# Performance work log

Hardware: AMD Instinct MI355X
Metric: run time of the kernel (lower is better)

Reference implementation:

```python
import jax, jax.numpy as jnp
import numpy as np

# Config (mirrors MarketBDHConfig / BDHConfig defaults used here)
B, T = 2, 512
NUM_ASSETS, IN_FEAT = 93, 4
D = 256          # n_embd
NH = 4           # n_head
MULT = 64        # mlp_internal_dim_multiplier
NL = 6           # n_layer
NI = D * MULT // NH  # per-head internal dim N = 4096
IN_DIM = NUM_ASSETS * IN_FEAT  # 372
ROPE_THETA = 2.0 ** 16
EPS = 1e-5


def _ln(x):
    # LayerNorm over last dim, elementwise_affine=False
    m = jnp.mean(x, axis=-1, keepdims=True)
    v = jnp.mean(jnp.square(x - m), axis=-1, keepdims=True)
    return (x - m) * jax.lax.rsqrt(v + EPS)


def _rope(x, cos, sin):
    # x: [B,NH,T,NI]; cos/sin: [T, NI//2] (broadcast over B,NH)
    x1, x2 = x[..., 0::2], x[..., 1::2]
    out = jnp.stack([x1 * cos - x2 * sin, x1 * sin + x2 * cos], axis=-1)
    return out.reshape(x.shape)


def setup_inputs() -> dict:
    key = jax.random.key(0)
    ks = jax.random.split(key, 9)
    s = 0.02
    return {
        "x": jax.random.normal(ks[0], (B, T, NUM_ASSETS, IN_FEAT), jnp.float32),
        "in_W": jax.random.normal(ks[1], (IN_DIM, D), jnp.float32) * s,
        "in_b": jnp.zeros((D,), jnp.float32),
        "encoder": jax.random.normal(ks[2], (NH, D, NI), jnp.float32) * s,
        "encoder_v": jax.random.normal(ks[3], (NH, D, NI), jnp.float32) * s,
        "decoder": jax.random.normal(ks[4], (NH * NI, D), jnp.float32) * s,
        "head_W": jax.random.normal(ks[5], (D, IN_DIM), jnp.float32) * s,
        "head_b": jnp.zeros((IN_DIM,), jnp.float32),
    }


def reference(x, in_W, in_b, encoder, encoder_v, decoder, head_W, head_b):
    # input projection: [B,T,N,F] -> [B,T,IN_DIM] -> [B,T,D]
    x_flat = x.reshape(B, T, IN_DIM)
    h = _ln(x_flat @ in_W + in_b)  # [B,T,D]

    # RoPE phase tables over the internal (latent) dimension
    freqs = 1.0 / (ROPE_THETA ** (jnp.arange(0, NI, 2, dtype=jnp.float32) / NI))
    phases = jnp.arange(T, dtype=jnp.float32)[:, None] * freqs[None, :]  # [T, NI/2]
    cos, sin = jnp.cos(phases), jnp.sin(phases)

    dec = decoder.reshape(NH, NI, D)  # head-major flatten matches transpose(1,2).reshape

    for _ in range(NL):
        h_res = h
        # encode + relu-sparsify: [B,NH,T,NI]
        h_sparse = jax.nn.relu(jnp.einsum('btd,hdn->bhtn', h, encoder))
        # BDH attention: linear (no softmax), K is Q, is_causal=False -> dense scores
        qr = _rope(h_sparse, cos, sin)
        scores = jnp.einsum('bhtn,bhsn->bhts', qr, qr)  # [B,NH,T,T]
        yKV = jnp.einsum('bhts,bsd->bhtd', scores, h)    # V = h broadcast over heads
        yKV = _ln(yKV)
        y_sparse = jax.nn.relu(jnp.einsum('bhtd,hdn->bhtn', yKV, encoder_v))
        xy_sparse = h_sparse * y_sparse  # multiplicative gating (dropout p=0)
        yMLP = jnp.einsum('bhtn,hnd->btd', xy_sparse, dec)
        h = _ln(h_res + _ln(yMLP))

    pred = (h @ head_W + head_b).reshape(B, T, NUM_ASSETS, IN_FEAT)
    return pred
```

## Files before the change

### kernel.cpp

```cpp
#include <hip/hip_runtime.h>
#include <math.h>

#define B_ 2
#define T_ 512
#define D_ 256
#define NH_ 4
#define NI_ 4096
#define IN_DIM_ 372
#define NL_ 6
#define EPS_ 1e-5f

typedef unsigned short u16;
typedef __attribute__((ext_vector_type(4))) float f32x4;
typedef __attribute__((ext_vector_type(8))) short bf16x8;

__device__ __forceinline__ u16 f2b(float f) {
  union { float f; unsigned u; } v; v.f = f;
  unsigned r = v.u + 0x7fffu + ((v.u >> 16) & 1u);
  return (u16)(r >> 16);
}
__device__ __forceinline__ float b2f(u16 s) {
  union { unsigned u; float f; } v; v.u = ((unsigned)s) << 16;
  return v.f;
}

__device__ __forceinline__ void gload16(const u16* g, u16* l) {
  __builtin_amdgcn_global_load_lds(
      (const __attribute__((address_space(1))) unsigned int*)g,
      (__attribute__((address_space(3))) unsigned int*)l, 16, 0, 0);
}

__device__ __forceinline__ float blkSum256(float v, float* sb4) {
  #pragma unroll
  for (int o = 32; o > 0; o >>= 1) v += __shfl_down(v, o, 64);
  int w = threadIdx.x >> 6;
  __syncthreads();
  if ((threadIdx.x & 63) == 0) sb4[w] = v;
  __syncthreads();
  return sb4[0] + sb4[1] + sb4[2] + sb4[3];
}

__device__ __forceinline__ void gemm128(const u16* __restrict__ A,
                                        const u16* __restrict__ Bt,
                                        int lda, int k0, int k1,
                                        int row0, int col0,
                                        u16* Als, u16* Bls,
                                        f32x4 acc[4][4]) {
  const int tid = threadIdx.x;
  const int lane = tid & 63;
  const int wv = tid >> 6;
  const int wr = (wv >> 1) << 6;
  const int wc = (wv & 1) << 6;
  const int frow = lane & 15;
  const int kg = lane >> 4;
  const int sw = frow & 7;
  #pragma unroll
  for (int m = 0; m < 4; m++)
    #pragma unroll
    for (int n = 0; n < 4; n++) {
      f32x4 z = {0.f, 0.f, 0.f, 0.f};
      acc[m][n] = z;
    }
  for (int k = k0; k < k1; k += 64) {
    #pragma unroll
    for (int i = 0; i < 4; i++) {
      int s = tid + (i << 8);
      int r = s >> 3;
      int c = (((s & 7) ^ (r & 7)) << 3);
      gload16(A + (long)(row0 + r) * lda + k + c, Als + s * 8);
      gload16(Bt + (long)(col0 + r) * lda + k + c, Bls + s * 8);
    }
    __syncthreads();
    #pragma unroll
    for (int kk = 0; kk < 2; kk++) {
      const int slot = ((((kk << 2) + kg) ^ sw) << 3);
      bf16x8 af[4], bfv[4];
      #pragma unroll
      for (int m = 0; m < 4; m++)
        af[m] = *(const bf16x8*)(Als + (wr + m * 16 + frow) * 64 + slot);
      #pragma unroll
      for (int n = 0; n < 4; n++)
        bfv[n] = *(const bf16x8*)(Bls + (wc + n * 16 + frow) * 64 + slot);
      #pragma unroll
      for (int m = 0; m < 4; m++)
        #pragma unroll
        for (int n = 0; n < 4; n++)
          acc[m][n] = __builtin_amdgcn_mfma_f32_16x16x32_bf16(af[m], bfv[n], acc[m][n], 0, 0, 0);
    }
    __syncthreads();
  }
}

#define EPILOG_SETUP \
  const int lane = threadIdx.x & 63; \
  const int wv = threadIdx.x >> 6; \
  const int wr = (wv >> 1) << 6, wc = (wv & 1) << 6;

#define STAGE_HALF(EXPR) \
  if (wr == h * 64) { \
    _Pragma("unroll") \
    for (int m = 0; m < 4; m++) \
      _Pragma("unroll") \
      for (int n = 0; n < 4; n++) \
        _Pragma("unroll") \
        for (int r = 0; r < 4; r++) { \
          int lr = m * 16 + ((lane >> 4) << 2) + r; \
          int lc = wc + n * 16 + (lane & 15); \
          float _a = acc[m][n][r]; \
          smem[lr * 128 + (lc ^ (((lr >> 2) & 7) << 3))] = f2b(EXPR); \
        } \
  } \
  __syncthreads();

__device__ __forceinline__ void storeC_lds(const f32x4 acc[4][4], u16* smem,
                                           u16* Cb, int ldc, int row0, int col0,
                                           int wr, int wc, int lane) {
  const int tid = threadIdx.x;
  #pragma unroll
  for (int h = 0; h < 2; h++) {
    STAGE_HALF(_a)
    #pragma unroll
    for (int i = 0; i < 4; i++) {
      int idx = i * 256 + tid;
      int lr = idx >> 4, ch = idx & 15;
      uint4 v = *(const uint4*)(smem + lr * 128 + ((ch ^ ((lr >> 2) & 7)) << 3));
      *(uint4*)(Cb + (long)(row0 + h * 64 + lr) * ldc + col0 + ch * 8) = v;
    }
    __syncthreads();
  }
}

__global__ __launch_bounds__(256)
void k_cs(unsigned* __restrict__ cs) {
  int idx = blockIdx.x * 256 + threadIdx.x;
  if (idx >= T_ * (NI_ / 2)) return;
  int t = idx >> 11;
  int k = idx & 2047;
  float freq = exp2f(-(float)k * (1.0f / 128.0f));
  float ph = (float)t * freq;
  cs[idx] = (unsigned)f2b(cosf(ph)) | ((unsigned)f2b(sinf(ph)) << 16);
}

__global__ __launch_bounds__(256)
void ktr(const float* __restrict__ src, u16* __restrict__ dst, int R, int C) {
  __shared__ float tile[64][65];
  long zoff = (long)blockIdx.z * R * C;
  int r0 = blockIdx.y * 64, c0 = blockIdx.x * 64;
  int tid = threadIdx.x;
  int tr = tid >> 4, tc4 = (tid & 15) * 4;
  #pragma unroll
  for (int i = 0; i < 4; i++) {
    int r = tr + i * 16;
    f32x4 v = *(const f32x4*)(src + zoff + (long)(r0 + r) * C + c0 + tc4);
    tile[r][tc4 + 0] = v.x; tile[r][tc4 + 1] = v.y;
    tile[r][tc4 + 2] = v.z; tile[r][tc4 + 3] = v.w;
  }
  __syncthreads();
  #pragma unroll
  for (int i = 0; i < 4; i++) {
    int c = tr + i * 16;
    ushort4 o;
    o.x = f2b(tile[tc4 + 0][c]); o.y = f2b(tile[tc4 + 1][c]);
    o.z = f2b(tile[tc4 + 2][c]); o.w = f2b(tile[tc4 + 3][c]);
    *(ushort4*)(dst + zoff + (long)(c0 + c) * R + r0 + tc4) = o;
  }
}

__global__ __launch_bounds__(256)
void k_input(const float* __restrict__ x, const float* __restrict__ W,
             const float* __restrict__ b, float* __restrict__ hf,
             u16* __restrict__ hbf, u16* __restrict__ hT) {
  __shared__ float xr[IN_DIM_];
  __shared__ float sb[4];
  int bt = blockIdx.x;
  int d = threadIdx.x;
  const float* xrow = x + (long)bt * IN_DIM_;
  for (int k = d; k < IN_DIM_; k += 256) xr[k] = xrow[k];
  __syncthreads();
  float acc = b[d];
  for (int k = 0; k < IN_DIM_; k++) acc += xr[k] * W[k * D_ + d];
  float mean = blkSum256(acc, sb) * (1.0f / D_);
  float c = acc - mean;
  float var = blkSum256(c * c, sb) * (1.0f / D_);
  float out = c * rsqrtf(var + EPS_);
  hf[(long)bt * D_ + d] = out;
  hbf[(long)bt * D_ + d] = f2b(out);
  hT[((long)(bt >> 9) * D_ + d) * T_ + (bt & 511)] = f2b(out);
}

__global__ __launch_bounds__(256)
void g_enc(const u16* __restrict__ hbf, const u16* __restrict__ enct,
           const unsigned* __restrict__ cs, u16* __restrict__ qr) {
  __shared__ u16 smem[16384];
  int head = blockIdx.z;
  int row0 = blockIdx.y * 128, col0 = blockIdx.x * 128;
  f32x4 acc[4][4];
  gemm128(hbf, enct + (long)head * NI_ * D_, D_, 0, D_, row0, col0,
          smem, smem + 8192, acc);
  EPILOG_SETUP
  const int tid = threadIdx.x;
  #pragma unroll
  for (int h = 0; h < 2; h++) {
    STAGE_HALF(fmaxf(_a, 0.f))
    #pragma unroll
    for (int i = 0; i < 4; i++) {
      int idx = i * 256 + tid;
      int lr = idx >> 4, ch = idx & 15;
      uint4 v = *(const uint4*)(smem + lr * 128 + ((ch ^ ((lr >> 2) & 7)) << 3));
      int gr = row0 + h * 64 + lr;
      int b = gr >> 9, t = gr & 511;
      int gcol = col0 + ch * 8;
      uint4 csv = *(const uint4*)(cs + (long)t * (NI_ / 2) + (gcol >> 1));
      const unsigned* pv = &v.x; const unsigned* pc = &csv.x;
      unsigned o[4];
      #pragma unroll
      for (int j = 0; j < 4; j++) {
        float v0 = b2f((u16)pv[j]), v1 = b2f((u16)(pv[j] >> 16));
        float cc = b2f((u16)pc[j]), ss = b2f((u16)(pc[j] >> 16));
        o[j] = (unsigned)f2b(v0 * cc - v1 * ss) | ((unsigned)f2b(v0 * ss + v1 * cc) << 16);
      }
      long qri = (((long)(b * NH_ + head)) * T_ + t) * NI_ + gcol;
      *(uint4*)(qr + qri) = make_uint4(o[0], o[1], o[2], o[3]);
    }
    __syncthreads();
  }
}

__global__ __launch_bounds__(256)
void g_scores(const u16* __restrict__ qr, u16* __restrict__ scpb) {
  __shared__ u16 smem[16384];
  int z2 = blockIdx.z;
  int z = z2 >> 2, ks = z2 & 3;
  const u16* A = qr + (long)z * T_ * NI_;
  int row0 = blockIdx.y * 128, col0 = blockIdx.x * 128;
  f32x4 acc[4][4];
  gemm128(A, A, NI_, ks * 1024, ks * 1024 + 1024, row0, col0,
          smem, smem + 8192, acc);
  EPILOG_SETUP
  storeC_lds(acc, smem, scpb + (long)(ks * 8 + z) * T_ * T_, T_, row0, col0, wr, wc, lane);
}

__global__ __launch_bounds__(256)
void g_ykv(const u16* __restrict__ scpb, const u16* __restrict__ hT,
           u16* __restrict__ ykvpb) {
  __shared__ u16 smem[16384];
  u16* Als = smem;
  u16* Bls = smem + 8192;
  int z2 = blockIdx.z;
  int z = z2 >> 2, ks = z2 & 3;
  int b = z >> 2;
  int row0 = blockIdx.y * 128, col0 = blockIdx.x * 128;
  const long SL = (long)8 * T_ * T_;
  const u16* Ab = scpb + (long)z * T_ * T_;
  const u16* Bt = hT + (long)b * D_ * T_;
  const int tid = threadIdx.x;
  const int lane = tid & 63;
  const int wv = tid >> 6;
  const int wr = (wv >> 1) << 6, wc = (wv & 1) << 6;
  const int frow = lane & 15;
  const int kg = lane >> 4;
  const int sw = frow & 7;
  f32x4 acc[4][4];
  #pragma unroll
  for (int m = 0; m < 4; m++)
    #pragma unroll
    for (int n = 0; n < 4; n++) {
      f32x4 zz = {0.f, 0.f, 0.f, 0.f};
      acc[m][n] = zz;
    }
  const int ar = tid >> 1;
  const int ac0 = (tid & 1) << 2;
  for (int k = ks * 128; k < ks * 128 + 128; k += 64) {
    long gb = (long)(row0 + ar) * T_ + k;
    #pragma unroll
    for (int j = 0; j < 4; j++) {
      int jj = ac0 + j;
      long ga = gb + (jj << 3);
      uint4 p0 = *(const uint4*)(Ab + ga);
      uint4 p1 = *(const uint4*)(Ab + SL + ga);
      uint4 p2 = *(const uint4*)(Ab + 2 * SL + ga);
      uint4 p3 = *(const uint4*)(Ab + 3 * SL + ga);
      const unsigned* q0 = &p0.x; const unsigned* q1 = &p1.x;
      const unsigned* q2 = &p2.x; const unsigned* q3 = &p3.x;
      unsigned o[4];
      #pragma unroll
      for (int w = 0; w < 4; w++) {
        float lo = b2f((u16)q0[w]) + b2f((u16)q1[w]) + b2f((u16)q2[w]) + b2f((u16)q3[w]);
        float hi = b2f((u16)(q0[w] >> 16)) + b2f((u16)(q1[w] >> 16)) +
                   b2f((u16)(q2[w] >> 16)) + b2f((u16)(q3[w] >> 16));
        o[w] = (unsigned)f2b(lo) | ((unsigned)f2b(hi) << 16);
      }
      *(uint4*)(Als + ar * 64 + ((jj ^ (ar & 7)) << 3)) = make_uint4(o[0], o[1], o[2], o[3]);
    }
    #pragma unroll
    for (int i = 0; i < 4; i++) {
      int s = tid + (i << 8);
      int r = s >> 3;
      int c = (((s & 7) ^ (r & 7)) << 3);
      gload16(Bt + (long)(col0 + r) * T_ + k + c, Bls + s * 8);
    }
    __syncthreads();
    #pragma unroll
    for (int kk = 0; kk < 2; kk++) {
      const int slot = ((((kk << 2) + kg) ^ sw) << 3);
      bf16x8 af[4], bfv[4];
      #pragma unroll
      for (int m = 0; m < 4; m++)
        af[m] = *(const bf16x8*)(Als + (wr + m * 16 + frow) * 64 + slot);
      #pragma unroll
      for (int n = 0; n < 4; n++)
        bfv[n] = *(const bf16x8*)(Bls + (wc + n * 16 + frow) * 64 + slot);
      #pragma unroll
      for (int m = 0; m < 4; m++)
        #pragma unroll
        for (int n = 0; n < 4; n++)
          acc[m][n] = __builtin_amdgcn_mfma_f32_16x16x32_bf16(af[m], bfv[n], acc[m][n], 0, 0, 0);
    }
    __syncthreads();
  }
  storeC_lds(acc, smem, ykvpb + (long)(ks * 8 + z) * T_ * D_, D_, row0, col0, wr, wc, lane);
}

__global__ __launch_bounds__(256)
void k_lnykv(const u16* __restrict__ ykvpb, u16* __restrict__ ykvb) {
  __shared__ float sb[4];
  int blk = blockIdx.x;
  int d = threadIdx.x;
  const long SL = (long)8 * T_ * D_;
  long base = (long)blk * D_ + d;
  float acc = b2f(ykvpb[base]) + b2f(ykvpb[SL + base]) +
              b2f(ykvpb[2 * SL + base]) + b2f(ykvpb[3 * SL + base]);
  float mean = blkSum256(acc, sb) * (1.0f / D_);
  float c = acc - mean;
  float var = blkSum256(c * c, sb) * (1.0f / D_);
  ykvb[base] = f2b(c * rsqrtf(var + EPS_));
}

__global__ __launch_bounds__(256)
void g_ysp(const u16* __restrict__ ykvb, const u16* __restrict__ encvt,
           const u16* __restrict__ qr, const unsigned* __restrict__ cs,
           u16* __restrict__ xy) {
  __shared__ u16 smem[16384];
  int z = blockIdx.z;
  int b = z >> 2, head = z & 3;
  int row0 = blockIdx.y * 128, col0 = blockIdx.x * 128;
  f32x4 acc[4][4];
  gemm128(ykvb + (long)z * T_ * D_, encvt + (long)head * NI_ * D_, D_,
          0, D_, row0, col0, smem, smem + 8192, acc);
  EPILOG_SETUP
  const int tid = threadIdx.x;
  #pragma unroll
  for (int h = 0; h < 2; h++) {
    STAGE_HALF(fmaxf(_a, 0.f))
    #pragma unroll
    for (int i = 0; i < 4; i++) {
      int idx = i * 256 + tid;
      int lr = idx >> 4, ch = idx & 15;
      uint4 v = *(const uint4*)(smem + lr * 128 + ((ch ^ ((lr >> 2) & 7)) << 3));
      int t = row0 + h * 64 + lr;
      int gcol = col0 + ch * 8;
      uint4 qv = *(const uint4*)(qr + ((long)z * T_ + t) * NI_ + gcol);
      uint4 csv = *(const uint4*)(cs + (long)t * (NI_ / 2) + (gcol >> 1));
      const unsigned* pv = &v.x; const unsigned* pq = &qv.x; const unsigned* pc = &csv.x;
      unsigned o[4];
      #pragma unroll
      for (int j = 0; j < 4; j++) {
        float v0 = b2f((u16)pv[j]), v1 = b2f((u16)(pv[j] >> 16));
        float q0 = b2f((u16)pq[j]), q1 = b2f((u16)(pq[j] >> 16));
        float cc = b2f((u16)pc[j]), ss = b2f((u16)(pc[j] >> 16));
        float hs0 = fmaxf(cc * q0 + ss * q1, 0.f);
        float hs1 = fmaxf(cc * q1 - ss * q0, 0.f);
        o[j] = (unsigned)f2b(hs0 * v0) | ((unsigned)f2b(hs1 * v1) << 16);
      }
      long xyi = ((long)b * T_ + t) * (NH_ * NI_) + head * NI_ + gcol;
      *(uint4*)(xy + xyi) = make_uint4(o[0], o[1], o[2], o[3]);
    }
    __syncthreads();
  }
}

__global__ __launch_bounds__(256)
void g_ymlp(const u16* __restrict__ xy, const u16* __restrict__ dect,
            u16* __restrict__ ymlppb) {
  __shared__ u16 smem[16384];
  int ks = blockIdx.z;
  int row0 = blockIdx.y * 128, col0 = blockIdx.x * 128;
  f32x4 acc[4][4];
  gemm128(xy, dect, NH_ * NI_, ks * 1024, ks * 1024 + 1024, row0, col0,
          smem, smem + 8192, acc);
  EPILOG_SETUP
  storeC_lds(acc, smem, ymlppb + (long)ks * (B_ * T_) * D_, D_, row0, col0, wr, wc, lane);
}

__global__ __launch_bounds__(256)
void k_dln(const u16* __restrict__ ymlppb, float* __restrict__ hf,
           u16* __restrict__ hbf, u16* __restrict__ hT) {
  __shared__ float sb[4];
  int bt = blockIdx.x;
  int d = threadIdx.x;
  const long SL = (long)(B_ * T_) * D_;
  float acc = 0.f;
  #pragma unroll
  for (int p = 0; p < 16; p++)
    acc += b2f(ymlppb[p * SL + (long)bt * D_ + d]);
  float mean = blkSum256(acc, sb) * (1.0f / D_);
  float c = acc - mean;
  float var = blkSum256(c * c, sb) * (1.0f / D_);
  float u = c * rsqrtf(var + EPS_);
  float v2 = hf[(long)bt * D_ + d] + u;
  float m2 = blkSum256(v2, sb) * (1.0f / D_);
  float c2 = v2 - m2;
  float va2 = blkSum256(c2 * c2, sb) * (1.0f / D_);
  float out = c2 * rsqrtf(va2 + EPS_);
  hf[(long)bt * D_ + d] = out;
  hbf[(long)bt * D_ + d] = f2b(out);
  hT[((long)(bt >> 9) * D_ + d) * T_ + (bt & 511)] = f2b(out);
}

__global__ __launch_bounds__(384)
void k_head(const float* __restrict__ h, const float* __restrict__ W,
            const float* __restrict__ bb, float* __restrict__ out) {
  __shared__ float hr[D_];
  int bt = blockIdx.x;
  int j = threadIdx.x;
  for (int k = j; k < D_; k += 384) hr[k] = h[(long)bt * D_ + k];
  __syncthreads();
  if (j < IN_DIM_) {
    float acc = bb[j];
    for (int d2 = 0; d2 < D_; d2++) acc += hr[d2] * W[(long)d2 * IN_DIM_ + j];
    out[(long)bt * IN_DIM_ + j] = acc;
  }
}

extern "C" void kernel_launch(void* const* d_in, const int* in_sizes, int n_in,
                              void* d_out, int out_size, void* d_ws, size_t ws_size,
                              hipStream_t stream) {
  const float* x    = (const float*)d_in[0];
  const float* in_W = (const float*)d_in[1];
  const float* in_b = (const float*)d_in[2];
  const float* enc  = (const float*)d_in[3];
  const float* encv = (const float*)d_in[4];
  const float* dec  = (const float*)d_in[5];
  const float* hW   = (const float*)d_in[6];
  const float* hb   = (const float*)d_in[7];
  float* out = (float*)d_out;

  char* p = (char*)d_ws;
  auto alloc = [&](size_t bytes) { char* r = p; p += (bytes + 255) & ~(size_t)255; return r; };
  unsigned* cs   = (unsigned*)alloc((size_t)T_ * (NI_ / 2) * 4);
  float* hf      = (float*)alloc((size_t)B_ * T_ * D_ * 4);
  u16*   hbf     = (u16*)  alloc((size_t)B_ * T_ * D_ * 2);
  u16*   hT      = (u16*)  alloc((size_t)B_ * D_ * T_ * 2);
  u16*   enct    = (u16*)  alloc((size_t)NH_ * D_ * NI_ * 2);
  u16*   encvt   = (u16*)  alloc((size_t)NH_ * D_ * NI_ * 2);
  u16*   dect    = (u16*)  alloc((size_t)NH_ * NI_ * D_ * 2);
  u16*   qr      = (u16*)  alloc((size_t)B_ * NH_ * T_ * NI_ * 2);
  u16*   xy      = (u16*)  alloc((size_t)B_ * T_ * NH_ * NI_ * 2);
  u16*   scpb    = (u16*)  alloc((size_t)4 * 8 * T_ * T_ * 2);
  u16*   ykvpb   = (u16*)  alloc((size_t)4 * 8 * T_ * D_ * 2);
  u16*   ykvb    = (u16*)  alloc((size_t)8 * T_ * D_ * 2);
  u16*   ymlppb  = (u16*)  alloc((size_t)16 * B_ * T_ * D_ * 2);

  k_cs<<<dim3(4096), dim3(256), 0, stream>>>(cs);
  ktr<<<dim3(NI_ / 64, D_ / 64, NH_), dim3(256), 0, stream>>>(enc, enct, D_, NI_);
  ktr<<<dim3(NI_ / 64, D_ / 64, NH_), dim3(256), 0, stream>>>(encv, encvt, D_, NI_);
  ktr<<<dim3(D_ / 64, (NH_ * NI_) / 64, 1), dim3(256), 0, stream>>>(dec, dect, NH_ * NI_, D_);
  k_input<<<dim3(B_ * T_), dim3(256), 0, stream>>>(x, in_W, in_b, hf, hbf, hT);

  for (int l = 0; l < NL_; l++) {
    g_enc<<<dim3(32, 8, 4), dim3(256), 0, stream>>>(hbf, enct, cs, qr);
    g_scores<<<dim3(4, 4, 32), dim3(256), 0, stream>>>(qr, scpb);
    g_ykv<<<dim3(2, 4, 32), dim3(256), 0, stream>>>(scpb, hT, ykvpb);
    k_lnykv<<<dim3(B_ * NH_ * T_), dim3(256), 0, stream>>>(ykvpb, ykvb);
    g_ysp<<<dim3(32, 4, 8), dim3(256), 0, stream>>>(ykvb, encvt, qr, cs, xy);
    g_ymlp<<<dim3(2, 8, 16), dim3(256), 0, stream>>>(xy, dect, ymlppb);
    k_dln<<<dim3(B_ * T_), dim3(256), 0, stream>>>(ymlppb, hf, hbf, hT);
  }

  k_head<<<dim3(B_ * T_), dim3(384), 0, stream>>>(hf, hW, hb, out);
}
```

Measured before the change: 798.4 us.

## Double-buffer GEMM LDS, exploit score symmetry, wave-level layernorms, merge transposes

The shared GEMM core now double-buffers its LDS tiles, issuing the next k-slice's global-to-LDS loads before computing on the current one. The scores GEMM computes only the upper-triangular 128x128 tiles of the symmetric Q·Qᵀ and writes each off-diagonal tile again in transposed form. The two layernorm kernels switch to one row per wavefront with vectorized loads and shuffle reductions, dropping block-level barriers. The two encoder weight transposes merge into one launch. Exchanges: doubled LDS per block, which may lower occupancy, and strided uncoalesced writes for the mirrored score tiles.

```diff
diff --git a/kernel.cpp b/kernel.cpp
--- a/kernel.cpp
+++ b/kernel.cpp
@@ -28,6 +28,12 @@
   __builtin_amdgcn_global_load_lds(
       (const __attribute__((address_space(1))) unsigned int*)g,
       (__attribute__((address_space(3))) unsigned int*)l, 16, 0, 0);
+}
+
+__device__ __forceinline__ float waveSum(float v) {
+  #pragma unroll
+  for (int o = 32; o > 0; o >>= 1) v += __shfl_xor(v, o, 64);
+  return v;
 }
 
 __device__ __forceinline__ float blkSum256(float v, float* sb4) {
@@ -61,26 +67,33 @@
       f32x4 z = {0.f, 0.f, 0.f, 0.f};
       acc[m][n] = z;
     }
-  for (int k = k0; k < k1; k += 64) {
+  auto stage = [&](int k, int buf) {
     #pragma unroll
     for (int i = 0; i < 4; i++) {
       int s = tid + (i << 8);
       int r = s >> 3;
       int c = (((s & 7) ^ (r & 7)) << 3);
-      gload16(A + (long)(row0 + r) * lda + k + c, Als + s * 8);
-      gload16(Bt + (long)(col0 + r) * lda + k + c, Bls + s * 8);
-    }
-    __syncthreads();
+      gload16(A + (long)(row0 + r) * lda + k + c, Als + buf * 8192 + s * 8);
+      gload16(Bt + (long)(col0 + r) * lda + k + c, Bls + buf * 8192 + s * 8);
+    }
+  };
+  stage(k0, 0);
+  __syncthreads();
+  int cur = 0;
+  for (int k = k0; k < k1; k += 64) {
+    if (k + 64 < k1) stage(k + 64, cur ^ 1);
+    const u16* Ab = Als + cur * 8192;
+    const u16* Bb = Bls + cur * 8192;
     #pragma unroll
     for (int kk = 0; kk < 2; kk++) {
       const int slot = ((((kk << 2) + kg) ^ sw) << 3);
       bf16x8 af[4], bfv[4];
       #pragma unroll
       for (int m = 0; m < 4; m++)
-        af[m] = *(const bf16x8*)(Als + (wr + m * 16 + frow) * 64 + slot);
+        af[m] = *(const bf16x8*)(Ab + (wr + m * 16 + frow) * 64 + slot);
       #pragma unroll
       for (int n = 0; n < 4; n++)
-        bfv[n] = *(const bf16x8*)(Bls + (wc + n * 16 + frow) * 64 + slot);
+        bfv[n] = *(const bf16x8*)(Bb + (wc + n * 16 + frow) * 64 + slot);
       #pragma unroll
       for (int m = 0; m < 4; m++)
         #pragma unroll
@@ -88,6 +101,7 @@
           acc[m][n] = __builtin_amdgcn_mfma_f32_16x16x32_bf16(af[m], bfv[n], acc[m][n], 0, 0, 0);
     }
     __syncthreads();
+    cur ^= 1;
   }
 }
 
@@ -167,6 +181,35 @@
 }
 
 __global__ __launch_bounds__(256)
+void ktrW(const float* __restrict__ e0, const float* __restrict__ e1,
+          u16* __restrict__ d0, u16* __restrict__ d1) {
+  __shared__ float tile[64][65];
+  int z = blockIdx.z;
+  const float* src = (z < 4) ? e0 : e1;
+  u16* dst = (z < 4) ? d0 : d1;
+  long zoff = (long)(z & 3) * D_ * NI_;
+  int r0 = blockIdx.y * 64, c0 = blockIdx.x * 64;
+  int tid = threadIdx.x;
+  int tr = tid >> 4, tc4 = (tid & 15) * 4;
+  #pragma unroll
+  for (int i = 0; i < 4; i++) {
+    int r = tr + i * 16;
+    f32x4 v = *(const f32x4*)(src + zoff + (long)(r0 + r) * NI_ + c0 + tc4);
+    tile[r][tc4 + 0] = v.x; tile[r][tc4 + 1] = v.y;
+    tile[r][tc4 + 2] = v.z; tile[r][tc4 + 3] = v.w;
+  }
+  __syncthreads();
+  #pragma unroll
+  for (int i = 0; i < 4; i++) {
+    int c = tr + i * 16;
+    ushort4 o;
+    o.x = f2b(tile[tc4 + 0][c]); o.y = f2b(tile[tc4 + 1][c]);
+    o.z = f2b(tile[tc4 + 2][c]); o.w = f2b(tile[tc4 + 3][c]);
+    *(ushort4*)(dst + zoff + (long)(c0 + c) * D_ + r0 + tc4) = o;
+  }
+}
+
+__global__ __launch_bounds__(256)
 void k_input(const float* __restrict__ x, const float* __restrict__ W,
              const float* __restrict__ b, float* __restrict__ hf,
              u16* __restrict__ hbf, u16* __restrict__ hT) {
@@ -191,12 +234,12 @@
 __global__ __launch_bounds__(256)
 void g_enc(const u16* __restrict__ hbf, const u16* __restrict__ enct,
            const unsigned* __restrict__ cs, u16* __restrict__ qr) {
-  __shared__ u16 smem[16384];
+  __shared__ u16 smem[32768];
   int head = blockIdx.z;
   int row0 = blockIdx.y * 128, col0 = blockIdx.x * 128;
   f32x4 acc[4][4];
   gemm128(hbf, enct + (long)head * NI_ * D_, D_, 0, D_, row0, col0,
-          smem, smem + 8192, acc);
+          smem, smem + 16384, acc);
   EPILOG_SETUP
   const int tid = threadIdx.x;
   #pragma unroll
@@ -228,16 +271,34 @@
 
 __global__ __launch_bounds__(256)
 void g_scores(const u16* __restrict__ qr, u16* __restrict__ scpb) {
-  __shared__ u16 smem[16384];
+  __shared__ u16 smem[32768];
+  int tix = blockIdx.x;
+  int by = (tix < 4) ? 0 : (tix < 7) ? 1 : (tix < 9) ? 2 : 3;
+  int sub = (by == 0) ? 0 : (by == 1) ? 3 : (by == 2) ? 5 : 6;
+  int bx = tix - sub;
   int z2 = blockIdx.z;
   int z = z2 >> 2, ks = z2 & 3;
   const u16* A = qr + (long)z * T_ * NI_;
-  int row0 = blockIdx.y * 128, col0 = blockIdx.x * 128;
+  int row0 = by * 128, col0 = bx * 128;
   f32x4 acc[4][4];
   gemm128(A, A, NI_, ks * 1024, ks * 1024 + 1024, row0, col0,
-          smem, smem + 8192, acc);
+          smem, smem + 16384, acc);
   EPILOG_SETUP
-  storeC_lds(acc, smem, scpb + (long)(ks * 8 + z) * T_ * T_, T_, row0, col0, wr, wc, lane);
+  u16* Cb = scpb + (long)(ks * 8 + z) * T_ * T_;
+  storeC_lds(acc, smem, Cb, T_, row0, col0, wr, wc, lane);
+  if (by != bx) {
+    #pragma unroll
+    for (int m = 0; m < 4; m++)
+      #pragma unroll
+      for (int n = 0; n < 4; n++) {
+        int gc = col0 + wc + n * 16 + (lane & 15);
+        int gr0 = row0 + wr + m * 16 + ((lane >> 4) << 2);
+        uint2 o;
+        o.x = (unsigned)f2b(acc[m][n][0]) | ((unsigned)f2b(acc[m][n][1]) << 16);
+        o.y = (unsigned)f2b(acc[m][n][2]) | ((unsigned)f2b(acc[m][n][3]) << 16);
+        *(uint2*)(Cb + (long)gc * T_ + gr0) = o;
+      }
+  }
 }
 
 __global__ __launch_bounds__(256)
@@ -323,30 +384,38 @@
 
 __global__ __launch_bounds__(256)
 void k_lnykv(const u16* __restrict__ ykvpb, u16* __restrict__ ykvb) {
-  __shared__ float sb[4];
-  int blk = blockIdx.x;
-  int d = threadIdx.x;
+  int row = blockIdx.x * 4 + (threadIdx.x >> 6);
+  int lane = threadIdx.x & 63;
   const long SL = (long)8 * T_ * D_;
-  long base = (long)blk * D_ + d;
-  float acc = b2f(ykvpb[base]) + b2f(ykvpb[SL + base]) +
-              b2f(ykvpb[2 * SL + base]) + b2f(ykvpb[3 * SL + base]);
-  float mean = blkSum256(acc, sb) * (1.0f / D_);
-  float c = acc - mean;
-  float var = blkSum256(c * c, sb) * (1.0f / D_);
-  ykvb[base] = f2b(c * rsqrtf(var + EPS_));
+  long base = (long)row * D_ + lane * 4;
+  float v0 = 0.f, v1 = 0.f, v2 = 0.f, v3 = 0.f;
+  #pragma unroll
+  for (int p = 0; p < 4; p++) {
+    uint2 w = *(const uint2*)(ykvpb + p * SL + base);
+    v0 += b2f((u16)w.x); v1 += b2f((u16)(w.x >> 16));
+    v2 += b2f((u16)w.y); v3 += b2f((u16)(w.y >> 16));
+  }
+  float mean = waveSum(v0 + v1 + v2 + v3) * (1.0f / D_);
+  float c0 = v0 - mean, c1 = v1 - mean, c2 = v2 - mean, c3 = v3 - mean;
+  float var = waveSum(c0 * c0 + c1 * c1 + c2 * c2 + c3 * c3) * (1.0f / D_);
+  float rs = rsqrtf(var + EPS_);
+  uint2 o;
+  o.x = (unsigned)f2b(c0 * rs) | ((unsigned)f2b(c1 * rs) << 16);
+  o.y = (unsigned)f2b(c2 * rs) | ((unsigned)f2b(c3 * rs) << 16);
+  *(uint2*)(ykvb + base) = o;
 }
 
 __global__ __launch_bounds__(256)
 void g_ysp(const u16* __restrict__ ykvb, const u16* __restrict__ encvt,
            const u16* __restrict__ qr, const unsigned* __restrict__ cs,
            u16* __restrict__ xy) {
-  __shared__ u16 smem[16384];
+  __shared__ u16 smem[32768];
   int z = blockIdx.z;
   int b = z >> 2, head = z & 3;
   int row0 = blockIdx.y * 128, col0 = blockIdx.x * 128;
   f32x4 acc[4][4];
   gemm128(ykvb + (long)z * T_ * D_, encvt + (long)head * NI_ * D_, D_,
-          0, D_, row0, col0, smem, smem + 8192, acc);
+          0, D_, row0, col0, smem, smem + 16384, acc);
   EPILOG_SETUP
   const int tid = threadIdx.x;
   #pragma unroll
@@ -382,12 +451,12 @@
 __global__ __launch_bounds__(256)
 void g_ymlp(const u16* __restrict__ xy, const u16* __restrict__ dect,
             u16* __restrict__ ymlppb) {
-  __shared__ u16 smem[16384];
+  __shared__ u16 smem[32768];
   int ks = blockIdx.z;
   int row0 = blockIdx.y * 128, col0 = blockIdx.x * 128;
   f32x4 acc[4][4];
   gemm128(xy, dect, NH_ * NI_, ks * 1024, ks * 1024 + 1024, row0, col0,
-          smem, smem + 8192, acc);
+          smem, smem + 16384, acc);
   EPILOG_SETUP
   storeC_lds(acc, smem, ymlppb + (long)ks * (B_ * T_) * D_, D_, row0, col0, wr, wc, lane);
 }
@@ -395,26 +464,41 @@
 __global__ __launch_bounds__(256)
 void k_dln(const u16* __restrict__ ymlppb, float* __restrict__ hf,
            u16* __restrict__ hbf, u16* __restrict__ hT) {
-  __shared__ float sb[4];
-  int bt = blockIdx.x;
-  int d = threadIdx.x;
+  int bt = blockIdx.x * 4 + (threadIdx.x >> 6);
+  int lane = threadIdx.x & 63;
   const long SL = (long)(B_ * T_) * D_;
-  float acc = 0.f;
-  #pragma unroll
-  for (int p = 0; p < 16; p++)
-    acc += b2f(ymlppb[p * SL + (long)bt * D_ + d]);
-  float mean = blkSum256(acc, sb) * (1.0f / D_);
-  float c = acc - mean;
-  float var = blkSum256(c * c, sb) * (1.0f / D_);
-  float u = c * rsqrtf(var + EPS_);
-  float v2 = hf[(long)bt * D_ + d] + u;
-  float m2 = blkSum256(v2, sb) * (1.0f / D_);
-  float c2 = v2 - m2;
-  float va2 = blkSum256(c2 * c2, sb) * (1.0f / D_);
-  float out = c2 * rsqrtf(va2 + EPS_);
-  hf[(long)bt * D_ + d] = out;
-  hbf[(long)bt * D_ + d] = f2b(out);
-  hT[((long)(bt >> 9) * D_ + d) * T_ + (bt & 511)] = f2b(out);
+  long base = (long)bt * D_ + lane * 4;
+  float v0 = 0.f, v1 = 0.f, v2 = 0.f, v3 = 0.f;
+  #pragma unroll
+  for (int p = 0; p < 16; p++) {
+    uint2 w = *(const uint2*)(ymlppb + p * SL + base);
+    v0 += b2f((u16)w.x); v1 += b2f((u16)(w.x >> 16));
+    v2 += b2f((u16)w.y); v3 += b2f((u16)(w.y >> 16));
+  }
+  float mean = waveSum(v0 + v1 + v2 + v3) * (1.0f / D_);
+  float c0 = v0 - mean, c1 = v1 - mean, c2 = v2 - mean, c3 = v3 - mean;
+  float var = waveSum(c0 * c0 + c1 * c1 + c2 * c2 + c3 * c3) * (1.0f / D_);
+  float rs = rsqrtf(var + EPS_);
+  f32x4 hv = *(const f32x4*)(hf + base);
+  float w0 = hv.x + c0 * rs, w1 = hv.y + c1 * rs;
+  float w2 = hv.z + c2 * rs, w3 = hv.w + c3 * rs;
+  float m2 = waveSum(w0 + w1 + w2 + w3) * (1.0f / D_);
+  float e0 = w0 - m2, e1 = w1 - m2, e2 = w2 - m2, e3 = w3 - m2;
+  float va2 = waveSum(e0 * e0 + e1 * e1 + e2 * e2 + e3 * e3) * (1.0f / D_);
+  float rs2 = rsqrtf(va2 + EPS_);
+  float o0 = e0 * rs2, o1 = e1 * rs2, o2 = e2 * rs2, o3 = e3 * rs2;
+  f32x4 of = {o0, o1, o2, o3};
+  *(f32x4*)(hf + base) = of;
+  uint2 ob;
+  ob.x = (unsigned)f2b(o0) | ((unsigned)f2b(o1) << 16);
+  ob.y = (unsigned)f2b(o2) | ((unsigned)f2b(o3) << 16);
+  *(uint2*)(hbf + base) = ob;
+  int b = bt >> 9, t = bt & 511;
+  int d0 = lane * 4;
+  hT[((long)b * D_ + d0 + 0) * T_ + t] = f2b(o0);
+  hT[((long)b * D_ + d0 + 1) * T_ + t] = f2b(o1);
+  hT[((long)b * D_ + d0 + 2) * T_ + t] = f2b(o2);
+  hT[((long)b * D_ + d0 + 3) * T_ + t] = f2b(o3);
 }
 
 __global__ __launch_bounds__(384)
@@ -462,19 +546,18 @@
   u16*   ymlppb  = (u16*)  alloc((size_t)16 * B_ * T_ * D_ * 2);
 
   k_cs<<<dim3(4096), dim3(256), 0, stream>>>(cs);
-  ktr<<<dim3(NI_ / 64, D_ / 64, NH_), dim3(256), 0, stream>>>(enc, enct, D_, NI_);
-  ktr<<<dim3(NI_ / 64, D_ / 64, NH_), dim3(256), 0, stream>>>(encv, encvt, D_, NI_);
+  ktrW<<<dim3(NI_ / 64, D_ / 64, 8), dim3(256), 0, stream>>>(enc, encv, enct, encvt);
   ktr<<<dim3(D_ / 64, (NH_ * NI_) / 64, 1), dim3(256), 0, stream>>>(dec, dect, NH_ * NI_, D_);
   k_input<<<dim3(B_ * T_), dim3(256), 0, stream>>>(x, in_W, in_b, hf, hbf, hT);
 
   for (int l = 0; l < NL_; l++) {
     g_enc<<<dim3(32, 8, 4), dim3(256), 0, stream>>>(hbf, enct, cs, qr);
-    g_scores<<<dim3(4, 4, 32), dim3(256), 0, stream>>>(qr, scpb);
+    g_scores<<<dim3(10, 1, 32), dim3(256), 0, stream>>>(qr, scpb);
     g_ykv<<<dim3(2, 4, 32), dim3(256), 0, stream>>>(scpb, hT, ykvpb);
-    k_lnykv<<<dim3(B_ * NH_ * T_), dim3(256), 0, stream>>>(ykvpb, ykvb);
+    k_lnykv<<<dim3(1024), dim3(256), 0, stream>>>(ykvpb, ykvb);
     g_ysp<<<dim3(32, 4, 8), dim3(256), 0, stream>>>(ykvb, encvt, qr, cs, xy);
     g_ymlp<<<dim3(2, 8, 16), dim3(256), 0, stream>>>(xy, dect, ymlppb);
-    k_dln<<<dim3(B_ * T_), dim3(256), 0, stream>>>(ymlppb, hf, hbf, hT);
+    k_dln<<<dim3(256), dim3(256), 0, stream>>>(ymlppb, hf, hbf, hT);
   }
 
   k_head<<<dim3(B_ * T_), dim3(384), 0, stream>>>(hf, hW, hb, out);
```

Measured after the change: 766.3 us. 4.0% less time.
